# Performance work log

Hardware: AMD Instinct MI355X
Metric: run time of the kernel (lower is better)

The kernel has to match this reference:

```python
import jax, jax.numpy as jnp
import numpy as np

GROUP_SIZE = 64
SHARED_EXPERT_WEIGHT = 1.0
# FP4 E2M1 codebook: sign bit + {0,.5,1,1.5,2,3,4,6}
FP4_TABLE = jnp.array([0.0, 0.5, 1.0, 1.5, 2.0, 3.0, 4.0, 6.0,
                       -0.0, -0.5, -1.0, -1.5, -2.0, -3.0, -4.0, -6.0], dtype=jnp.float32)


def dequant_fp4(packed, scales, group_size=GROUP_SIZE):
    """packed: [..., K//8, N] int32 (8 nibbles along K per word),
    scales: [..., K//group_size, N] -> dequantized [..., K, N] fp32."""
    shifts = (jnp.arange(8, dtype=jnp.int32) * 4)[:, None]          # [8,1]
    nib = jnp.right_shift(packed[..., :, None, :], shifts) & 0xF     # [..., K//8, 8, N]
    w = FP4_TABLE[nib]
    K = packed.shape[-2] * 8
    w = w.reshape(packed.shape[:-2] + (K, packed.shape[-1]))         # [..., K, N]
    s = jnp.repeat(scales, group_size, axis=-2)                      # [..., K, N]
    return w * s


def setup_inputs() -> dict:
    key = jax.random.key(0)
    ks = jax.random.split(key, 12)
    T, K, I, E, TOPK = 2048, 2048, 1024, 8, 2
    GS = GROUP_SIZE
    MAXI = 2**31 - 1
    u = lambda k, shp: jax.random.uniform(k, shp, jnp.float32, 0.005, 0.02)
    probs = jax.random.uniform(ks[10], (T, TOPK), jnp.float32)
    probs = probs / probs.sum(-1, keepdims=True)
    return {
        "hidden_states": jax.random.normal(ks[0], (T, K), jnp.float32),
        "gate_up_weight_packed": jax.random.randint(ks[1], (E, K // 8, 2 * I), 0, MAXI, jnp.int32),
        "gate_up_scales": u(ks[2], (E, K // GS, 2 * I)),
        "down_weight_packed": jax.random.randint(ks[3], (E, I // 8, K), 0, MAXI, jnp.int32),
        "down_scales": u(ks[4], (E, I // GS, K)),
        "shared_gate_up_packed": jax.random.randint(ks[5], (K // 8, 2 * I), 0, MAXI, jnp.int32),
        "shared_gate_up_scales": u(ks[6], (K // GS, 2 * I)),
        "shared_down_packed": jax.random.randint(ks[7], (I // 8, K), 0, MAXI, jnp.int32),
        "shared_down_scales": u(ks[8], (I // GS, K)),
        "expert_ids": jax.random.randint(ks[9], (T, TOPK), 0, E, jnp.int32),
        "expert_probs": probs,
    }


def reference(hidden_states, gate_up_weight_packed, gate_up_scales,
              down_weight_packed, down_scales,
              shared_gate_up_packed, shared_gate_up_scales,
              shared_down_packed, shared_down_scales,
              expert_ids, expert_probs):
    x = hidden_states                                                # [T, K]
    E = gate_up_weight_packed.shape[0]
    # --- routed experts: dequant + grouped GEMM over all tokens per expert ---
    Wgu = dequant_fp4(gate_up_weight_packed, gate_up_scales)         # [E, K, 2I]
    Wd = dequant_fp4(down_weight_packed, down_scales)                # [E, I, K]
    h = jnp.einsum('tk,ekn->etn', x, Wgu)                            # [E, T, 2I]
    gate, up = jnp.split(h, 2, axis=-1)
    act = jax.nn.silu(gate) * up                                     # [E, T, I]
    y = jnp.einsum('eti,eik->etk', act, Wd)                          # [E, T, K]
    # combine[t,e] = sum over top-k slots routed to e of prob
    one_hot = jax.nn.one_hot(expert_ids, E, dtype=x.dtype)           # [T, topk, E]
    combine = jnp.einsum('tk,tke->te', expert_probs, one_hot)        # [T, E]
    out = jnp.einsum('te,etk->tk', combine, y)                       # [T, K]
    # --- shared expert (always applied, weighted) ---
    Wgu_s = dequant_fp4(shared_gate_up_packed, shared_gate_up_scales)  # [K, 2I]
    Wd_s = dequant_fp4(shared_down_packed, shared_down_scales)         # [I, K]
    hs = x @ Wgu_s
    gs, us = jnp.split(hs, 2, axis=-1)
    shared_out = (jax.nn.silu(gs) * us) @ Wd_s
    return out + SHARED_EXPERT_WEIGHT * shared_out
```

## Files before the change

### kernel.cpp

```cpp
#include <hip/hip_runtime.h>
#include <hip/hip_bf16.h>

#define T_TOK 2048
#define K_DIM 2048
#define I_DIM 1024
#define NE    8
#define TOPK  2
#define GS    64

#define NSLOT  (T_TOK * TOPK)
#define TOTROW (NSLOT + T_TOK)
#define MAXITEM 32
#define DQD_Y   72

typedef __attribute__((ext_vector_type(8))) short short8;
typedef __attribute__((ext_vector_type(4))) float f32x4;

#define WS_XB   ((size_t)65536)
#define WS_ACT  (WS_XB  + (size_t)2048 * 2048 * 2)
#define WS_Y    (WS_ACT + (size_t)TOTROW * 1024 * 2)
#define WS_WGU  (WS_Y   + (size_t)TOTROW * 2048 * 2)
#define WS_WD   (WS_WGU + (size_t)9 * 2048 * 2048 * 2)


__device__ __forceinline__ unsigned pack2(float a, float b) {
    __hip_bfloat162 h = __float22bfloat162_rn(make_float2(a, b));
    return *reinterpret_cast<unsigned*>(&h);
}

__device__ __forceinline__ unsigned scale2(unsigned p, float s) {
    float f0 = __uint_as_float(p << 16) * s;
    float f1 = __uint_as_float(p & 0xFFFF0000u) * s;
    return pack2(f0, f1);
}

__device__ __forceinline__ float bf2f(ushort h) {
    return __uint_as_float((unsigned)h << 16);
}

__device__ __forceinline__ void dq_word(unsigned w, float s, unsigned o[4]) {
    unsigned lo  = w & 0x0F0F0F0Fu;
    unsigned hi  = (w >> 4) & 0x0F0F0F0Fu;
    unsigned mlo = lo & 0x07070707u, mhi = hi & 0x07070707u;
    unsigned Hlo = __builtin_amdgcn_perm(0x40404040u, 0x3F3F3F00u, mlo);
    unsigned Hhi = __builtin_amdgcn_perm(0x40404040u, 0x3F3F3F00u, mhi);
    unsigned Llo = __builtin_amdgcn_perm(0xC0804000u, 0xC0800000u, mlo);
    unsigned Lhi = __builtin_amdgcn_perm(0xC0804000u, 0xC0800000u, mhi);
    Hlo |= (lo & 0x08080808u) << 4;
    Hhi |= (hi & 0x08080808u) << 4;
    unsigned e01 = __builtin_amdgcn_perm(Hlo, Llo, 0x05010400u);
    unsigned e23 = __builtin_amdgcn_perm(Hlo, Llo, 0x07030602u);
    unsigned o01 = __builtin_amdgcn_perm(Hhi, Lhi, 0x05010400u);
    unsigned o23 = __builtin_amdgcn_perm(Hhi, Lhi, 0x07030602u);
    o[0] = scale2(e01, s); o[1] = scale2(e23, s);
    o[2] = scale2(o01, s); o[3] = scale2(o23, s);
}

__device__ __forceinline__ void dq4(const int* __restrict__ wp, const float* __restrict__ sc,
                                    ushort* __restrict__ op, int KW, int kb, int nb, int tid) {
    const int N = 2048;
    int n   = nb * 64 + (tid & 63);
    int kwt = kb * 16 + (tid >> 6) * 4;
    float s = sc[(size_t)(kwt >> 3) * N + n];
    ushort* dst = op + (size_t)n * (KW * 8) + kwt * 8;
    #pragma unroll
    for (int j = 0; j < 4; j++) {
        unsigned w = (unsigned)wp[(size_t)(kwt + j) * N + n];
        unsigned o[4]; dq_word(w, s, o);
        *(int4*)(dst + j * 8) = make_int4(o[0], o[1], o[2], o[3]);
    }
}

__device__ __forceinline__ void gld16(const void* g, void* l) {
    __builtin_amdgcn_global_load_lds(
        (const __attribute__((address_space(1))) unsigned*)g,
        (__attribute__((address_space(3))) unsigned*)l, 16, 0, 0);
}

#define GU_BLK  (9 * 512)
#define PREP_BLK 2048
#define FRONT_GRID (GU_BLK + PREP_BLK + 1)

__global__ __launch_bounds__(256) void k_front(
        const float* __restrict__ x, ushort* __restrict__ xb,
        const int* __restrict__ gup, const float* __restrict__ gus,
        const int* __restrict__ sup, const float* __restrict__ sus,
        ushort* __restrict__ wgu_t,
        const int* __restrict__ eids, const float* __restrict__ probs,
        int* __restrict__ gcnt, int* __restrict__ gbase,
        int* __restrict__ tileCnt, int* __restrict__ tileE, int* __restrict__ tileM,
        int* __restrict__ tok, int* __restrict__ inv) {
    int id = blockIdx.x;
    int tid = threadIdx.x;

    if (id < GU_BLK) {
        int e = id >> 9, rem = id & 511;
        int kb = rem & 15, nb = rem >> 4;
        const int* wp; const float* sc;
        if (e < NE) { wp = gup + (size_t)e * 256 * 2048; sc = gus + (size_t)e * 32 * 2048; }
        else        { wp = sup; sc = sus; }
        dq4(wp, sc, wgu_t + (size_t)e * 2048 * 2048, 256, kb, nb, tid);
    } else if (id < GU_BLK + PREP_BLK) {
        int idx = (id - GU_BLK) * 256 + tid;
        const float4* p = (const float4*)(x + (size_t)idx * 8);
        float4 f0 = p[0], f1 = p[1];
        unsigned u0 = pack2(f0.x, f0.z);
        unsigned u1 = pack2(f1.x, f1.z);
        unsigned u2 = pack2(f0.y, f0.w);
        unsigned u3 = pack2(f1.y, f1.w);
        *(int4*)(xb + (size_t)idx * 8) = make_int4(u0, u1, u2, u3);
    } else {
        __shared__ int lcnt[NE], lbase[NE], lcur[NE];
        if (tid < NE) lcnt[tid] = 0;
        __syncthreads();
        for (int i = tid; i < NSLOT; i += 256)
            atomicAdd(&lcnt[eids[i]], 1);
        __syncthreads();
        if (tid == 0) {
            int acc = 0;
            for (int e = 0; e < NE; e++) { lbase[e] = acc; acc += lcnt[e]; }
        }
        __syncthreads();
        if (tid < NE) lcur[tid] = lbase[tid];
        __syncthreads();
        for (int i = tid; i < NSLOT; i += 256) {
            int e = eids[i];
            int pos = atomicAdd(&lcur[e], 1);
            tok[pos] = i >> 1;
            inv[i] = pos;
        }
        for (int t = tid; t < T_TOK; t += 256)
            tok[NSLOT + t] = t;
        if (tid < NE) { gcnt[tid] = lcnt[tid]; gbase[tid] = lbase[tid]; }
        if (tid == 0) {
            gcnt[NE] = T_TOK; gbase[NE] = NSLOT;
            int nt = 0;
            for (int e = 0; e < NE + 1; e++) {
                int c = (e < NE) ? lcnt[e] : T_TOK;
                for (int m = 0; m < c; m += 256) { tileE[nt] = e; tileM[nt] = m; nt++; }
            }
            *tileCnt = nt;
            for (int i = nt; i < 64; i++) { tileE[i] = 0; tileM[i] = 0; }
        }
    }
}

__global__ __launch_bounds__(1024) void k_gemm_gateup(
        const ushort* __restrict__ xb, const ushort* __restrict__ wgu_t,
        const int* __restrict__ dwp, const float* __restrict__ dsc,
        const int* __restrict__ sdp, const float* __restrict__ sds,
        ushort* __restrict__ wd_t,
        const int* __restrict__ gcnt, const int* __restrict__ gbase,
        const int* __restrict__ tileCnt, const int* __restrict__ tileE,
        const int* __restrict__ tileM,
        const int* __restrict__ tokid, ushort* __restrict__ act) {
    int tid = threadIdx.x;
    if (blockIdx.y >= MAXITEM) {
        int id2 = ((blockIdx.y - MAXITEM) * 8 + blockIdx.x) * 4 + (tid >> 8);
        int e = id2 >> 8, rem = id2 & 255;
        int kb = rem & 7, nbl = rem >> 3;
        const int* wp; const float* sc;
        if (e < NE) { wp = dwp + (size_t)e * 128 * 2048; sc = dsc + (size_t)e * 16 * 2048; }
        else        { wp = sdp; sc = sds; }
        dq4(wp, sc, wd_t + (size_t)e * 2048 * 1024, 128, kb, nbl, tid & 255);
        return;
    }
    int item = blockIdx.y;
    if (item >= *tileCnt) return;
    int e = tileE[item], m0 = tileM[item];
    int cnt = gcnt[e], base = gbase[e];
    int n0 = blockIdx.x * 128;
    const ushort* wt = wgu_t + (size_t)e * 2048 * K_DIM;

    __shared__ __align__(16) ushort xs[256 * 64];
    __shared__ __align__(16) ushort bs[256 * 64];

    int lane = tid & 63, wv = tid >> 6;
    int lid = lane & 15, quad = lane >> 4;
    int wr = wv >> 2, wc = wv & 3;
    int l8 = lane >> 3, l7 = lane & 7;
    int chunk = (l7 ^ l8) * 8;

    const ushort* aSrc[2]; const ushort* bSrc[2];
    #pragma unroll
    for (int it = 0; it < 2; it++) {
        int rA = wv * 16 + it * 8 + l8;
        int t = (m0 + rA < cnt) ? tokid[base + m0 + rA] : 0;
        aSrc[it] = xb + (size_t)t * K_DIM + chunk;
        int h = rA >> 6, j = rA & 63;
        int col = (j < 32) ? (n0 + h * 32 + j) : (I_DIM + n0 + h * 32 + (j - 32));
        bSrc[it] = wt + (size_t)col * K_DIM + chunk;
    }

    f32x4 acc[4][4] = {};

    for (int k0 = 0; k0 < K_DIM; k0 += 64) {
        #pragma unroll
        for (int it = 0; it < 2; it++) {
            gld16(aSrc[it] + k0, &xs[(wv * 2 + it) * 512]);
            gld16(bSrc[it] + k0, &bs[(wv * 2 + it) * 512]);
        }
        __syncthreads();
        #pragma unroll
        for (int ks = 0; ks < 2; ks++) {
            int slot = ((ks * 4 + quad) ^ l7) * 8;
            short8 a[4], b[4];
            #pragma unroll
            for (int mt = 0; mt < 4; mt++)
                a[mt] = *(const short8*)&xs[(wr * 64 + mt * 16 + lid) * 64 + slot];
            #pragma unroll
            for (int nt = 0; nt < 4; nt++)
                b[nt] = *(const short8*)&bs[(wc * 64 + nt * 16 + lid) * 64 + slot];
            #pragma unroll
            for (int mt = 0; mt < 4; mt++)
                #pragma unroll
                for (int nt = 0; nt < 4; nt++)
                    acc[mt][nt] = __builtin_amdgcn_mfma_f32_16x16x32_bf16(
                        a[mt], b[nt], acc[mt][nt], 0, 0, 0);
        }
        __syncthreads();
    }

    int c7 = lid & 7;
    int delta = ((c7 >> 1) + ((c7 & 1) << 2)) - c7;
    #pragma unroll
    for (int mt = 0; mt < 4; mt++) {
        #pragma unroll
        for (int i = 0; i < 4; i++) {
            int row = wr * 64 + mt * 16 + quad * 4 + i;
            if (m0 + row < cnt) {
                size_t p = (size_t)(base + m0 + row);
                #pragma unroll
                for (int nt = 0; nt < 2; nt++) {
                    float g = acc[mt][nt][i], u = acc[mt][nt + 2][i];
                    float vv = g / (1.f + __expf(-g)) * u;
                    int ncol = n0 + wc * 32 + nt * 16 + lid;
                    __hip_bfloat16 hb = __float2bfloat16(vv);
                    act[p * I_DIM + ncol + delta] = *reinterpret_cast<ushort*>(&hb);
                }
            }
        }
    }
}

__global__ __launch_bounds__(1024) void k_gemm_down(
        const ushort* __restrict__ actb, const ushort* __restrict__ wd_t,
        const int* __restrict__ gcnt, const int* __restrict__ gbase,
        const int* __restrict__ tileCnt, const int* __restrict__ tileE,
        const int* __restrict__ tileM,
        ushort* __restrict__ y) {
    int item = blockIdx.y;
    if (item >= *tileCnt) return;
    int e = tileE[item], m0 = tileM[item];
    int cnt = gcnt[e], base = gbase[e];
    int n0 = blockIdx.x * 256;
    const ushort* wt = wd_t + (size_t)e * 2048 * I_DIM;

    __shared__ __align__(16) ushort xs[256 * 64];
    __shared__ __align__(16) ushort bs[256 * 64];

    int tid = threadIdx.x;
    int lane = tid & 63, wv = tid >> 6;
    int lid = lane & 15, quad = lane >> 4;
    int wr = wv >> 2, wc = wv & 3;
    int l8 = lane >> 3, l7 = lane & 7;
    int chunk = (l7 ^ l8) * 8;

    const ushort* aSrc[2]; const ushort* bSrc[2];
    #pragma unroll
    for (int it = 0; it < 2; it++) {
        int rA = wv * 16 + it * 8 + l8;
        int rr = m0 + rA; if (rr >= cnt) rr = cnt - 1;
        aSrc[it] = actb + (size_t)(base + rr) * I_DIM + chunk;
        bSrc[it] = wt + (size_t)(n0 + rA) * I_DIM + chunk;
    }

    f32x4 acc[4][4] = {};

    for (int i0 = 0; i0 < I_DIM; i0 += 64) {
        #pragma unroll
        for (int it = 0; it < 2; it++) {
            gld16(aSrc[it] + i0, &xs[(wv * 2 + it) * 512]);
            gld16(bSrc[it] + i0, &bs[(wv * 2 + it) * 512]);
        }
        __syncthreads();
        #pragma unroll
        for (int ks = 0; ks < 2; ks++) {
            int slot = ((ks * 4 + quad) ^ l7) * 8;
            short8 a[4], b[4];
            #pragma unroll
            for (int mt = 0; mt < 4; mt++)
                a[mt] = *(const short8*)&xs[(wr * 64 + mt * 16 + lid) * 64 + slot];
            #pragma unroll
            for (int nt = 0; nt < 4; nt++)
                b[nt] = *(const short8*)&bs[(wc * 64 + nt * 16 + lid) * 64 + slot];
            #pragma unroll
            for (int mt = 0; mt < 4; mt++)
                #pragma unroll
                for (int nt = 0; nt < 4; nt++)
                    acc[mt][nt] = __builtin_amdgcn_mfma_f32_16x16x32_bf16(
                        a[mt], b[nt], acc[mt][nt], 0, 0, 0);
        }
        __syncthreads();
    }

    #pragma unroll
    for (int mt = 0; mt < 4; mt++) {
        #pragma unroll
        for (int i = 0; i < 4; i++) {
            int row = wr * 64 + mt * 16 + quad * 4 + i;
            if (m0 + row < cnt) {
                ushort* yrow = y + (size_t)(base + m0 + row) * 2048 + n0 + wc * 64 + lid;
                #pragma unroll
                for (int nt = 0; nt < 4; nt++) {
                    __hip_bfloat16 hb = __float2bfloat16(acc[mt][nt][i]);
                    yrow[nt * 16] = *reinterpret_cast<ushort*>(&hb);
                }
            }
        }
    }
}

__global__ __launch_bounds__(256) void k_combine(
        const ushort* __restrict__ y, const int* __restrict__ inv,
        const float* __restrict__ prb, float* __restrict__ out) {
    int idx = blockIdx.x * 256 + threadIdx.x;
    int t = idx >> 8;
    int c = (idx & 255) * 8;
    int p0 = inv[2 * t], p1 = inv[2 * t + 1];
    float w0 = prb[2 * t], w1 = prb[2 * t + 1];
    int4 a = *(const int4*)(y + (size_t)p0 * 2048 + c);
    int4 b = *(const int4*)(y + (size_t)p1 * 2048 + c);
    int4 s = *(const int4*)(y + (size_t)(NSLOT + t) * 2048 + c);
    const ushort* au = (const ushort*)&a;
    const ushort* bu = (const ushort*)&b;
    const ushort* su = (const ushort*)&s;
    float o[8];
    #pragma unroll
    for (int j = 0; j < 8; j++)
        o[j] = w0 * bf2f(au[j]) + w1 * bf2f(bu[j]) + bf2f(su[j]);
    *(float4*)(out + (size_t)t * 2048 + c)     = *(float4*)&o[0];
    *(float4*)(out + (size_t)t * 2048 + c + 4) = *(float4*)&o[4];
}

extern "C" void kernel_launch(void* const* d_in, const int* in_sizes, int n_in,
                              void* d_out, int out_size, void* d_ws, size_t ws_size,
                              hipStream_t stream) {
    const float* x    = (const float*)d_in[0];
    const int*   gup  = (const int*)d_in[1];
    const float* gus  = (const float*)d_in[2];
    const int*   dwp  = (const int*)d_in[3];
    const float* dsc  = (const float*)d_in[4];
    const int*   sup  = (const int*)d_in[5];
    const float* sus  = (const float*)d_in[6];
    const int*   sdp  = (const int*)d_in[7];
    const float* sds  = (const float*)d_in[8];
    const int*   eids = (const int*)d_in[9];
    const float* prb  = (const float*)d_in[10];
    float* out = (float*)d_out;

    char*   ws      = (char*)d_ws;
    int*    gcnt    = (int*)(ws + 0);
    int*    gbase   = (int*)(ws + 64);
    int*    tileCnt = (int*)(ws + 128);
    int*    tileE   = (int*)(ws + 192);
    int*    tileM   = (int*)(ws + 448);
    int*    tok     = (int*)(ws + 1024);
    int*    inv     = (int*)(ws + 25600);
    ushort* xb      = (ushort*)(ws + WS_XB);
    ushort* act     = (ushort*)(ws + WS_ACT);
    ushort* y       = (ushort*)(ws + WS_Y);
    ushort* wgu_t   = (ushort*)(ws + WS_WGU);
    ushort* wd_t    = (ushort*)(ws + WS_WD);

    k_front<<<FRONT_GRID, 256, 0, stream>>>(
        x, xb, gup, gus, sup, sus, wgu_t,
        eids, prb, gcnt, gbase, tileCnt, tileE, tileM, tok, inv);
    k_gemm_gateup<<<dim3(I_DIM / 128, MAXITEM + DQD_Y), 1024, 0, stream>>>(
        xb, wgu_t, dwp, dsc, sdp, sds, wd_t,
        gcnt, gbase, tileCnt, tileE, tileM, tok, act);
    k_gemm_down<<<dim3(K_DIM / 256, MAXITEM), 1024, 0, stream>>>(
        act, wd_t, gcnt, gbase, tileCnt, tileE, tileM, y);
    k_combine<<<(T_TOK * K_DIM / 8) / 256, 256, 0, stream>>>(y, inv, prb, out);
}
```

Baseline: 241.4 us.

## Fuse FP4 weight dequantization into GEMM B-tile loading

Removes the separate pass that dequantized all expert and shared weights to bf16 in global memory. Each GEMM block now reads packed FP4 words and scales directly, dequantizes them in registers into the swizzled LDS B tile, and prefetches the next k-step's words. This drops the large bf16 weight write and re-read traffic and the extra dequant blocks. In exchange, each M-tile block repeats the dequant work and the B path uses synchronous register loads instead of async global-to-LDS copies.

```diff
diff --git a/kernel.cpp b/kernel.cpp
--- a/kernel.cpp
+++ b/kernel.cpp
@@ -11,7 +11,6 @@
 #define NSLOT  (T_TOK * TOPK)
 #define TOTROW (NSLOT + T_TOK)
 #define MAXITEM 32
-#define DQD_Y   72
 
 typedef __attribute__((ext_vector_type(8))) short short8;
 typedef __attribute__((ext_vector_type(4))) float f32x4;
@@ -19,8 +18,6 @@
 #define WS_XB   ((size_t)65536)
 #define WS_ACT  (WS_XB  + (size_t)2048 * 2048 * 2)
 #define WS_Y    (WS_ACT + (size_t)TOTROW * 1024 * 2)
-#define WS_WGU  (WS_Y   + (size_t)TOTROW * 2048 * 2)
-#define WS_WD   (WS_WGU + (size_t)9 * 2048 * 2048 * 2)
 
 
 __device__ __forceinline__ unsigned pack2(float a, float b) {
@@ -56,52 +53,26 @@
     o[2] = scale2(o01, s); o[3] = scale2(o23, s);
 }
 
-__device__ __forceinline__ void dq4(const int* __restrict__ wp, const float* __restrict__ sc,
-                                    ushort* __restrict__ op, int KW, int kb, int nb, int tid) {
-    const int N = 2048;
-    int n   = nb * 64 + (tid & 63);
-    int kwt = kb * 16 + (tid >> 6) * 4;
-    float s = sc[(size_t)(kwt >> 3) * N + n];
-    ushort* dst = op + (size_t)n * (KW * 8) + kwt * 8;
-    #pragma unroll
-    for (int j = 0; j < 4; j++) {
-        unsigned w = (unsigned)wp[(size_t)(kwt + j) * N + n];
-        unsigned o[4]; dq_word(w, s, o);
-        *(int4*)(dst + j * 8) = make_int4(o[0], o[1], o[2], o[3]);
-    }
-}
-
 __device__ __forceinline__ void gld16(const void* g, void* l) {
     __builtin_amdgcn_global_load_lds(
         (const __attribute__((address_space(1))) unsigned*)g,
         (__attribute__((address_space(3))) unsigned*)l, 16, 0, 0);
 }
 
-#define GU_BLK  (9 * 512)
 #define PREP_BLK 2048
-#define FRONT_GRID (GU_BLK + PREP_BLK + 1)
+#define FRONT_GRID (PREP_BLK + 1)
 
 __global__ __launch_bounds__(256) void k_front(
         const float* __restrict__ x, ushort* __restrict__ xb,
-        const int* __restrict__ gup, const float* __restrict__ gus,
-        const int* __restrict__ sup, const float* __restrict__ sus,
-        ushort* __restrict__ wgu_t,
-        const int* __restrict__ eids, const float* __restrict__ probs,
+        const int* __restrict__ eids,
         int* __restrict__ gcnt, int* __restrict__ gbase,
         int* __restrict__ tileCnt, int* __restrict__ tileE, int* __restrict__ tileM,
         int* __restrict__ tok, int* __restrict__ inv) {
     int id = blockIdx.x;
     int tid = threadIdx.x;
 
-    if (id < GU_BLK) {
-        int e = id >> 9, rem = id & 511;
-        int kb = rem & 15, nb = rem >> 4;
-        const int* wp; const float* sc;
-        if (e < NE) { wp = gup + (size_t)e * 256 * 2048; sc = gus + (size_t)e * 32 * 2048; }
-        else        { wp = sup; sc = sus; }
-        dq4(wp, sc, wgu_t + (size_t)e * 2048 * 2048, 256, kb, nb, tid);
-    } else if (id < GU_BLK + PREP_BLK) {
-        int idx = (id - GU_BLK) * 256 + tid;
+    if (id < PREP_BLK) {
+        int idx = id * 256 + tid;
         const float4* p = (const float4*)(x + (size_t)idx * 8);
         float4 f0 = p[0], f1 = p[1];
         unsigned u0 = pack2(f0.x, f0.z);
@@ -146,31 +117,22 @@
 }
 
 __global__ __launch_bounds__(1024) void k_gemm_gateup(
-        const ushort* __restrict__ xb, const ushort* __restrict__ wgu_t,
-        const int* __restrict__ dwp, const float* __restrict__ dsc,
-        const int* __restrict__ sdp, const float* __restrict__ sds,
-        ushort* __restrict__ wd_t,
+        const ushort* __restrict__ xb,
+        const int* __restrict__ gup, const float* __restrict__ gus,
+        const int* __restrict__ sup, const float* __restrict__ sus,
         const int* __restrict__ gcnt, const int* __restrict__ gbase,
         const int* __restrict__ tileCnt, const int* __restrict__ tileE,
         const int* __restrict__ tileM,
         const int* __restrict__ tokid, ushort* __restrict__ act) {
-    int tid = threadIdx.x;
-    if (blockIdx.y >= MAXITEM) {
-        int id2 = ((blockIdx.y - MAXITEM) * 8 + blockIdx.x) * 4 + (tid >> 8);
-        int e = id2 >> 8, rem = id2 & 255;
-        int kb = rem & 7, nbl = rem >> 3;
-        const int* wp; const float* sc;
-        if (e < NE) { wp = dwp + (size_t)e * 128 * 2048; sc = dsc + (size_t)e * 16 * 2048; }
-        else        { wp = sdp; sc = sds; }
-        dq4(wp, sc, wd_t + (size_t)e * 2048 * 1024, 128, kb, nbl, tid & 255);
-        return;
-    }
     int item = blockIdx.y;
     if (item >= *tileCnt) return;
+    int tid = threadIdx.x;
     int e = tileE[item], m0 = tileM[item];
     int cnt = gcnt[e], base = gbase[e];
     int n0 = blockIdx.x * 128;
-    const ushort* wt = wgu_t + (size_t)e * 2048 * K_DIM;
+    const int* wp; const float* sc;
+    if (e < NE) { wp = gup + (size_t)e * 256 * 2048; sc = gus + (size_t)e * 32 * 2048; }
+    else        { wp = sup; sc = sus; }
 
     __shared__ __align__(16) ushort xs[256 * 64];
     __shared__ __align__(16) ushort bs[256 * 64];
@@ -181,24 +143,43 @@
     int l8 = lane >> 3, l7 = lane & 7;
     int chunk = (l7 ^ l8) * 8;
 
-    const ushort* aSrc[2]; const ushort* bSrc[2];
+    const ushort* aSrc[2];
     #pragma unroll
     for (int it = 0; it < 2; it++) {
         int rA = wv * 16 + it * 8 + l8;
         int t = (m0 + rA < cnt) ? tokid[base + m0 + rA] : 0;
         aSrc[it] = xb + (size_t)t * K_DIM + chunk;
-        int h = rA >> 6, j = rA & 63;
-        int col = (j < 32) ? (n0 + h * 32 + j) : (I_DIM + n0 + h * 32 + (j - 32));
-        bSrc[it] = wt + (size_t)col * K_DIM + chunk;
-    }
+    }
+
+    int nloc = tid & 255;
+    int kw0 = (tid >> 8) * 2;
+    int bj = nloc & 63, bh = nloc >> 6;
+    int ncol = (bj < 32) ? (n0 + bh * 32 + bj) : (I_DIM + n0 + bh * 32 + (bj - 32));
+    ushort* bd0 = &bs[nloc * 64 + ((kw0    ) ^ (nloc & 7)) * 8];
+    ushort* bd1 = &bs[nloc * 64 + ((kw0 + 1) ^ (nloc & 7)) * 8];
+
+    float s   = sc[ncol];
+    unsigned w0 = (unsigned)wp[(size_t)(kw0    ) * 2048 + ncol];
+    unsigned w1 = (unsigned)wp[(size_t)(kw0 + 1) * 2048 + ncol];
 
     f32x4 acc[4][4] = {};
 
     for (int k0 = 0; k0 < K_DIM; k0 += 64) {
         #pragma unroll
-        for (int it = 0; it < 2; it++) {
+        for (int it = 0; it < 2; it++)
             gld16(aSrc[it] + k0, &xs[(wv * 2 + it) * 512]);
-            gld16(bSrc[it] + k0, &bs[(wv * 2 + it) * 512]);
+        {
+            unsigned o[4];
+            dq_word(w0, s, o);
+            *(int4*)bd0 = make_int4(o[0], o[1], o[2], o[3]);
+            dq_word(w1, s, o);
+            *(int4*)bd1 = make_int4(o[0], o[1], o[2], o[3]);
+        }
+        int kn = k0 + 64;
+        if (kn < K_DIM) {
+            s  = sc[(size_t)(kn >> 6) * 2048 + ncol];
+            w0 = (unsigned)wp[(size_t)((kn >> 3) + kw0    ) * 2048 + ncol];
+            w1 = (unsigned)wp[(size_t)((kn >> 3) + kw0 + 1) * 2048 + ncol];
         }
         __syncthreads();
         #pragma unroll
@@ -234,9 +215,9 @@
                 for (int nt = 0; nt < 2; nt++) {
                     float g = acc[mt][nt][i], u = acc[mt][nt + 2][i];
                     float vv = g / (1.f + __expf(-g)) * u;
-                    int ncol = n0 + wc * 32 + nt * 16 + lid;
+                    int ncol2 = n0 + wc * 32 + nt * 16 + lid;
                     __hip_bfloat16 hb = __float2bfloat16(vv);
-                    act[p * I_DIM + ncol + delta] = *reinterpret_cast<ushort*>(&hb);
+                    act[p * I_DIM + ncol2 + delta] = *reinterpret_cast<ushort*>(&hb);
                 }
             }
         }
@@ -244,44 +225,68 @@
 }
 
 __global__ __launch_bounds__(1024) void k_gemm_down(
-        const ushort* __restrict__ actb, const ushort* __restrict__ wd_t,
+        const ushort* __restrict__ actb,
+        const int* __restrict__ dwp, const float* __restrict__ dsc,
+        const int* __restrict__ sdp, const float* __restrict__ sds,
         const int* __restrict__ gcnt, const int* __restrict__ gbase,
         const int* __restrict__ tileCnt, const int* __restrict__ tileE,
         const int* __restrict__ tileM,
         ushort* __restrict__ y) {
     int item = blockIdx.y;
     if (item >= *tileCnt) return;
+    int tid = threadIdx.x;
     int e = tileE[item], m0 = tileM[item];
     int cnt = gcnt[e], base = gbase[e];
     int n0 = blockIdx.x * 256;
-    const ushort* wt = wd_t + (size_t)e * 2048 * I_DIM;
+    const int* wp; const float* sc;
+    if (e < NE) { wp = dwp + (size_t)e * 128 * 2048; sc = dsc + (size_t)e * 16 * 2048; }
+    else        { wp = sdp; sc = sds; }
 
     __shared__ __align__(16) ushort xs[256 * 64];
     __shared__ __align__(16) ushort bs[256 * 64];
 
-    int tid = threadIdx.x;
     int lane = tid & 63, wv = tid >> 6;
     int lid = lane & 15, quad = lane >> 4;
     int wr = wv >> 2, wc = wv & 3;
     int l8 = lane >> 3, l7 = lane & 7;
     int chunk = (l7 ^ l8) * 8;
 
-    const ushort* aSrc[2]; const ushort* bSrc[2];
+    const ushort* aSrc[2];
     #pragma unroll
     for (int it = 0; it < 2; it++) {
         int rA = wv * 16 + it * 8 + l8;
         int rr = m0 + rA; if (rr >= cnt) rr = cnt - 1;
         aSrc[it] = actb + (size_t)(base + rr) * I_DIM + chunk;
-        bSrc[it] = wt + (size_t)(n0 + rA) * I_DIM + chunk;
-    }
+    }
+
+    int nloc = tid & 255;
+    int kw0 = (tid >> 8) * 2;
+    int ncol = n0 + nloc;
+    ushort* bd0 = &bs[nloc * 64 + ((kw0    ) ^ (nloc & 7)) * 8];
+    ushort* bd1 = &bs[nloc * 64 + ((kw0 + 1) ^ (nloc & 7)) * 8];
+
+    float s   = sc[ncol];
+    unsigned w0 = (unsigned)wp[(size_t)(kw0    ) * 2048 + ncol];
+    unsigned w1 = (unsigned)wp[(size_t)(kw0 + 1) * 2048 + ncol];
 
     f32x4 acc[4][4] = {};
 
     for (int i0 = 0; i0 < I_DIM; i0 += 64) {
         #pragma unroll
-        for (int it = 0; it < 2; it++) {
+        for (int it = 0; it < 2; it++)
             gld16(aSrc[it] + i0, &xs[(wv * 2 + it) * 512]);
-            gld16(bSrc[it] + i0, &bs[(wv * 2 + it) * 512]);
+        {
+            unsigned o[4];
+            dq_word(w0, s, o);
+            *(int4*)bd0 = make_int4(o[0], o[1], o[2], o[3]);
+            dq_word(w1, s, o);
+            *(int4*)bd1 = make_int4(o[0], o[1], o[2], o[3]);
+        }
+        int in0 = i0 + 64;
+        if (in0 < I_DIM) {
+            s  = sc[(size_t)(in0 >> 6) * 2048 + ncol];
+            w0 = (unsigned)wp[(size_t)((in0 >> 3) + kw0    ) * 2048 + ncol];
+            w1 = (unsigned)wp[(size_t)((in0 >> 3) + kw0 + 1) * 2048 + ncol];
         }
         __syncthreads();
         #pragma unroll
@@ -370,16 +375,12 @@
     ushort* xb      = (ushort*)(ws + WS_XB);
     ushort* act     = (ushort*)(ws + WS_ACT);
     ushort* y       = (ushort*)(ws + WS_Y);
-    ushort* wgu_t   = (ushort*)(ws + WS_WGU);
-    ushort* wd_t    = (ushort*)(ws + WS_WD);
 
     k_front<<<FRONT_GRID, 256, 0, stream>>>(
-        x, xb, gup, gus, sup, sus, wgu_t,
-        eids, prb, gcnt, gbase, tileCnt, tileE, tileM, tok, inv);
-    k_gemm_gateup<<<dim3(I_DIM / 128, MAXITEM + DQD_Y), 1024, 0, stream>>>(
-        xb, wgu_t, dwp, dsc, sdp, sds, wd_t,
-        gcnt, gbase, tileCnt, tileE, tileM, tok, act);
+        x, xb, eids, gcnt, gbase, tileCnt, tileE, tileM, tok, inv);
+    k_gemm_gateup<<<dim3(I_DIM / 128, MAXITEM), 1024, 0, stream>>>(
+        xb, gup, gus, sup, sus, gcnt, gbase, tileCnt, tileE, tileM, tok, act);
     k_gemm_down<<<dim3(K_DIM / 256, MAXITEM), 1024, 0, stream>>>(
-        act, wd_t, gcnt, gbase, tileCnt, tileE, tileM, y);
+        act, dwp, dsc, sdp, sds, gcnt, gbase, tileCnt, tileE, tileM, y);
     k_combine<<<(T_TOK * K_DIM / 8) / 256, 256, 0, stream>>>(y, inv, prb, out);
 }
```

After: 242.7 us. About the same (+0.5%).
